# Kernel tuning notes

Hardware: AMD Instinct MI355X
Metric: run time of the kernel (lower is better)

## Reference

```python
import jax, jax.numpy as jnp
import numpy as np

B, N, D_OBJ, D_Q, D_FUSED, D_BOX, D_ATT = 64, 36, 2048, 2048, 2048, 4, 512


def setup_inputs() -> dict:
    key = jax.random.key(0)
    ks = jax.random.split(key, 12)
    s = lambda d: 1.0 / np.sqrt(d)
    return {
        "question_embedding": jax.random.normal(ks[0], (B * N, D_Q), jnp.float32),
        "object_features_list": jax.random.normal(ks[1], (B, N, D_OBJ), jnp.float32),
        "bounding_boxes": jax.random.uniform(ks[2], (B, N, D_BOX), jnp.float32),
        "Wq": jax.random.normal(ks[3], (D_Q, D_FUSED), jnp.float32) * s(D_Q),
        "Wo": jax.random.normal(ks[4], (D_OBJ, D_FUSED), jnp.float32) * s(D_OBJ),
        "Wfa": jax.random.normal(ks[5], (D_FUSED, D_FUSED), jnp.float32) * s(D_FUSED),
        "Wfb": jax.random.normal(ks[6], (D_FUSED, D_FUSED), jnp.float32) * s(D_FUSED),
        "Wba": jax.random.normal(ks[7], (D_BOX, D_FUSED), jnp.float32) * s(D_BOX),
        "Wbb": jax.random.normal(ks[8], (D_BOX, D_FUSED), jnp.float32) * s(D_BOX),
        "W0": jax.random.normal(ks[9], (D_FUSED, D_ATT), jnp.float32) * s(D_FUSED),
        "b0": jnp.zeros((D_ATT,), jnp.float32),
        "W1": jax.random.normal(ks[10], (D_ATT, 1), jnp.float32) * s(D_ATT),
        "b1": jnp.zeros((1,), jnp.float32),
        "batch_size": B,
        "num_obj": N,
    }


def reference(question_embedding, object_features_list, bounding_boxes,
              Wq, Wo, Wfa, Wfb, Wba, Wbb, W0, b0, W1, b1,
              batch_size, num_obj):
    # fuse_object_features_with_questions: MLB fusion of question and objects
    obj_flat = object_features_list.reshape(batch_size * num_obj, -1)  # [BN, D]
    fused = (question_embedding @ Wq) * (obj_flat @ Wo)                # [BN, Df]
    fused = fused.reshape(batch_size, num_obj, -1)                     # [B, N, Df]

    # pairwise: project once, broadcast-multiply instead of materializing
    # expanded [B*N*N, D] operands (same math as expand+view+fusion).
    ra = fused @ Wfa                 # [B, N, Df]
    rb = fused @ Wfb                 # [B, N, Df]
    ba = bounding_boxes @ Wba        # [B, N, Df]
    bb = bounding_boxes @ Wbb        # [B, N, Df]
    # relations[b, i, j, :] = fusion_fused(f_i, f_j) + fusion_box(box_i, box_j)
    relations = ra[:, :, None, :] * rb[:, None, :, :] + ba[:, :, None, :] * bb[:, None, :, :]  # [B,N,N,Df]

    # compute_relation_attention: linear-tanh-linear, softmax over dim=2
    h = jnp.tanh(relations @ W0 + b0)          # [B, N, N, D_att]
    scores = h @ W1 + b1                       # [B, N, N, 1]
    att = jax.nn.softmax(scores, axis=2)[..., 0]  # [B, N, N]
    e_hat = jnp.sum(relations * att[..., None], axis=2)  # [B, N, Df]

    pairwise_res = fused + e_hat
    return object_features_list + pairwise_res
```

## Files before the change

kernel.cpp:

```cpp
#include <hip/hip_runtime.h>
#include <hip/hip_bf16.h>
#include <math.h>

constexpr int kB    = 64;
constexpr int kN    = 36;
constexpr int kBN   = kB * kN;
constexpr int kD    = 2048;
constexpr int kDatt = 512;
constexpr int kPairs = kN * kN;

using bf16x8 = __attribute__((ext_vector_type(8))) short;
using f32x4  = __attribute__((ext_vector_type(4))) float;

typedef unsigned int u32;
typedef __attribute__((address_space(3))) u32 lds_u32;
typedef const __attribute__((address_space(1))) u32 glb_u32;

__device__ inline unsigned short f2bf(float f) {
    union { float f; unsigned u; } v; v.f = f;
    unsigned r = v.u + 0x7FFFu + ((v.u >> 16) & 1u);
    return (unsigned short)(r >> 16);
}

__global__ __launch_bounds__(256)
void kcvt(const float* __restrict__ x, unsigned short* __restrict__ y, int n4)
{
    int i = blockIdx.x * 256 + threadIdx.x;
    if (i < n4) {
        float4 v = ((const float4*)x)[i];
        ushort4 o = {f2bf(v.x), f2bf(v.y), f2bf(v.z), f2bf(v.w)};
        ((ushort4*)y)[i] = o;
    }
}

__global__ __launch_bounds__(256)
void kzero(float* __restrict__ p, int n)
{
    int i = blockIdx.x * 256 + threadIdx.x;
    if (i < n) p[i] = 0.f;
}

__global__ __launch_bounds__(256)
void ktrp(const float* __restrict__ W, unsigned short* __restrict__ WT, int nt)
{
    __shared__ float T[64][65];
    const int k0 = blockIdx.x * 64;
    const int n0 = blockIdx.y * 64;
    const int c = threadIdx.x & 63, r0 = threadIdx.x >> 6;
    #pragma unroll
    for (int rr = 0; rr < 64; rr += 4)
        T[r0 + rr][c] = W[(size_t)(k0 + r0 + rr) * nt + n0 + c];
    __syncthreads();
    #pragma unroll
    for (int rr = 0; rr < 64; rr += 4)
        WT[(size_t)(n0 + r0 + rr) * kD + k0 + c] = f2bf(T[c][r0 + rr]);
}

__global__ __launch_bounds__(64)
void krepack_w0(const unsigned short* __restrict__ W0T, unsigned short* __restrict__ W0s)
{
    const int kb    = blockIdx.x;
    const int chunk = blockIdx.y;
    const int g     = threadIdx.x;
    const int row = chunk * 16 + (g & 7) + ((g >> 5) << 3);
    const int cg8 = ((g >> 3) & 3) * 8;
    const uint4 v = *(const uint4*)&W0T[(size_t)row * kD + kb * 32 + cg8];
    *(uint4*)&W0s[(size_t)kb * 16384 + chunk * 512 + g * 8] = v;
}

__global__ __launch_bounds__(256)
void kgbox(const float* __restrict__ Wba, const float* __restrict__ Wbb,
           const float* __restrict__ W0, float* __restrict__ Gpart)
{
    __shared__ float red[4][64][17];
    const int ct = blockIdx.x;
    const int kc = blockIdx.y;
    const int cl = threadIdx.x & 63;
    const int kq = threadIdx.x >> 6;
    const int c  = ct * 64 + cl;

    float acc[16];
    #pragma unroll
    for (int t = 0; t < 16; ++t) acc[t] = 0.f;

    const int kbase = kc * 128 + kq * 32;
    for (int kk = 0; kk < 32; ++kk) {
        int k = kbase + kk;
        float w0 = W0[(size_t)k * kDatt + c];
        float a0 = Wba[k], a1 = Wba[kD + k], a2 = Wba[2 * kD + k], a3 = Wba[3 * kD + k];
        float b0 = Wbb[k] * w0, b1 = Wbb[kD + k] * w0,
              b2 = Wbb[2 * kD + k] * w0, b3 = Wbb[3 * kD + k] * w0;
        acc[0]  = fmaf(a0, b0, acc[0]);  acc[1]  = fmaf(a0, b1, acc[1]);
        acc[2]  = fmaf(a0, b2, acc[2]);  acc[3]  = fmaf(a0, b3, acc[3]);
        acc[4]  = fmaf(a1, b0, acc[4]);  acc[5]  = fmaf(a1, b1, acc[5]);
        acc[6]  = fmaf(a1, b2, acc[6]);  acc[7]  = fmaf(a1, b3, acc[7]);
        acc[8]  = fmaf(a2, b0, acc[8]);  acc[9]  = fmaf(a2, b1, acc[9]);
        acc[10] = fmaf(a2, b2, acc[10]); acc[11] = fmaf(a2, b3, acc[11]);
        acc[12] = fmaf(a3, b0, acc[12]); acc[13] = fmaf(a3, b1, acc[13]);
        acc[14] = fmaf(a3, b2, acc[14]); acc[15] = fmaf(a3, b3, acc[15]);
    }
    #pragma unroll
    for (int t = 0; t < 16; ++t) red[kq][cl][t] = acc[t];
    __syncthreads();
    #pragma unroll
    for (int t = 0; t < 4; ++t) {
        int s = threadIdx.x + t * 256;
        int cc = s >> 4, uv = s & 15;
        float v = red[0][cc][uv] + red[1][cc][uv] + red[2][cc][uv] + red[3][cc][uv];
        Gpart[((size_t)kc * 16 + uv) * kDatt + ct * 64 + cc] = v;
    }
}

__global__ __launch_bounds__(64)
void krepack_g(const float* __restrict__ Gpart, unsigned short* __restrict__ W0s)
{
    const int chunk = blockIdx.x;
    const int g     = threadIdx.x;
    const int col = chunk * 16 + (g & 7) + ((g >> 5) << 3);
    const int kg  = (g >> 3) & 3;
    unsigned short o[8];
    #pragma unroll
    for (int e = 0; e < 8; ++e) {
        int kl = kg * 8 + e;
        if (kl < 16) {
            float s = 0.f;
            #pragma unroll
            for (int kc = 0; kc < 16; ++kc)
                s += Gpart[((size_t)kc * 16 + kl) * kDatt + col];
            o[e] = f2bf(s);
        } else o[e] = 0;
    }
    *(uint4*)&W0s[(size_t)64 * 16384 + chunk * 512 + g * 8] = *(uint4*)o;
}

__device__ inline void stage128(const unsigned short* __restrict__ g,
                                int grow0, int k0,
                                unsigned short* lds, int w, int lane)
{
    const int sr = lane >> 2, sc = (lane & 3) * 8;
    #pragma unroll
    for (int t = 0; t < 2; ++t) {
        int r = w * 32 + t * 16;
        const unsigned short* gp = g + (size_t)(grow0 + r + sr) * kD + k0 + sc;
        __builtin_amdgcn_global_load_lds((glb_u32*)gp, (lds_u32*)(lds + r * 32), 16, 0, 0);
    }
}
__device__ inline void stage64(const unsigned short* __restrict__ g,
                               int grow0, int k0,
                               unsigned short* lds, int w, int lane)
{
    const int sr = lane >> 2, sc = (lane & 3) * 8;
    int r = w * 16;
    const unsigned short* gp = g + (size_t)(grow0 + r + sr) * kD + k0 + sc;
    __builtin_amdgcn_global_load_lds((glb_u32*)gp, (lds_u32*)(lds + r * 32), 16, 0, 0);
}

__global__ __launch_bounds__(256, 2)
void k1_dual_mfma(const unsigned short* __restrict__ Qb,
                  const unsigned short* __restrict__ WqT,
                  const unsigned short* __restrict__ Ob,
                  const unsigned short* __restrict__ WoT,
                  unsigned short* __restrict__ fusedb)
{
    __shared__ __align__(16) unsigned short As1[128][32];
    __shared__ __align__(16) unsigned short As2[128][32];
    __shared__ __align__(16) unsigned short Bs1[64][32];
    __shared__ __align__(16) unsigned short Bs2[64][32];

    const int tid = threadIdx.x;
    const int lane = tid & 63;
    const int w = tid >> 6;
    const int wm = w >> 1, wn = w & 1;
    const int row0 = blockIdx.y * 128;
    const int col0 = blockIdx.x * 64;

    f32x4 acc1[4][2], acc2[4][2];
    #pragma unroll
    for (int mt = 0; mt < 4; ++mt)
        #pragma unroll
        for (int nt = 0; nt < 2; ++nt) { acc1[mt][nt] = (f32x4)(0.f); acc2[mt][nt] = (f32x4)(0.f); }

    const int fr = lane & 15, ko = (lane >> 4) * 8;

    for (int k0 = 0; k0 < kD; k0 += 32) {
        stage128(Qb,  row0, k0, &As1[0][0], w, lane);
        stage128(Ob,  row0, k0, &As2[0][0], w, lane);
        stage64 (WqT, col0, k0, &Bs1[0][0], w, lane);
        stage64 (WoT, col0, k0, &Bs2[0][0], w, lane);
        __syncthreads();

        bf16x8 a1[4], a2[4];
        #pragma unroll
        for (int mt = 0; mt < 4; ++mt) {
            a1[mt] = *(bf16x8*)&As1[wm * 64 + mt * 16 + fr][ko];
            a2[mt] = *(bf16x8*)&As2[wm * 64 + mt * 16 + fr][ko];
        }
        #pragma unroll
        for (int nt = 0; nt < 2; ++nt) {
            bf16x8 b1 = *(bf16x8*)&Bs1[wn * 32 + nt * 16 + fr][ko];
            bf16x8 b2 = *(bf16x8*)&Bs2[wn * 32 + nt * 16 + fr][ko];
            #pragma unroll
            for (int mt = 0; mt < 4; ++mt) {
                acc1[mt][nt] = __builtin_amdgcn_mfma_f32_16x16x32_bf16(a1[mt], b1, acc1[mt][nt], 0, 0, 0);
                acc2[mt][nt] = __builtin_amdgcn_mfma_f32_16x16x32_bf16(a2[mt], b2, acc2[mt][nt], 0, 0, 0);
            }
        }
        __syncthreads();
    }

    const int fq = lane >> 4;
    #pragma unroll
    for (int mt = 0; mt < 4; ++mt)
        #pragma unroll
        for (int nt = 0; nt < 2; ++nt) {
            int row = row0 + wm * 64 + mt * 16 + fq * 4;
            int col = col0 + wn * 32 + nt * 16 + fr;
            #pragma unroll
            for (int reg = 0; reg < 4; ++reg) {
                float v = acc1[mt][nt][reg] * acc2[mt][nt][reg];
                fusedb[(size_t)(row + reg) * kD + col] = f2bf(v);
            }
        }
}

__global__ __launch_bounds__(256, 2)
void k2_dual_mfma(const unsigned short* __restrict__ Fb,
                  const unsigned short* __restrict__ WfaT,
                  const unsigned short* __restrict__ WfbT,
                  float* __restrict__ ra, float* __restrict__ rb)
{
    __shared__ __align__(16) unsigned short As [128][32];
    __shared__ __align__(16) unsigned short Bs1[64][32];
    __shared__ __align__(16) unsigned short Bs2[64][32];

    const int tid = threadIdx.x;
    const int lane = tid & 63;
    const int w = tid >> 6;
    const int wm = w >> 1, wn = w & 1;
    const int row0 = blockIdx.y * 128;
    const int col0 = blockIdx.x * 64;

    f32x4 acc1[4][2], acc2[4][2];
    #pragma unroll
    for (int mt = 0; mt < 4; ++mt)
        #pragma unroll
        for (int nt = 0; nt < 2; ++nt) { acc1[mt][nt] = (f32x4)(0.f); acc2[mt][nt] = (f32x4)(0.f); }

    const int fr = lane & 15, ko = (lane >> 4) * 8;

    for (int k0 = 0; k0 < kD; k0 += 32) {
        stage128(Fb,   row0, k0, &As [0][0], w, lane);
        stage64 (WfaT, col0, k0, &Bs1[0][0], w, lane);
        stage64 (WfbT, col0, k0, &Bs2[0][0], w, lane);
        __syncthreads();

        bf16x8 a[4];
        #pragma unroll
        for (int mt = 0; mt < 4; ++mt)
            a[mt] = *(bf16x8*)&As[wm * 64 + mt * 16 + fr][ko];
        #pragma unroll
        for (int nt = 0; nt < 2; ++nt) {
            bf16x8 b1 = *(bf16x8*)&Bs1[wn * 32 + nt * 16 + fr][ko];
            bf16x8 b2 = *(bf16x8*)&Bs2[wn * 32 + nt * 16 + fr][ko];
            #pragma unroll
            for (int mt = 0; mt < 4; ++mt) {
                acc1[mt][nt] = __builtin_amdgcn_mfma_f32_16x16x32_bf16(a[mt], b1, acc1[mt][nt], 0, 0, 0);
                acc2[mt][nt] = __builtin_amdgcn_mfma_f32_16x16x32_bf16(a[mt], b2, acc2[mt][nt], 0, 0, 0);
            }
        }
        __syncthreads();
    }

    const int fq = lane >> 4;
    #pragma unroll
    for (int mt = 0; mt < 4; ++mt)
        #pragma unroll
        for (int nt = 0; nt < 2; ++nt) {
            int row = row0 + wm * 64 + mt * 16 + fq * 4;
            int col = col0 + wn * 32 + nt * 16 + fr;
            #pragma unroll
            for (int reg = 0; reg < 4; ++reg) {
                size_t o = (size_t)(row + reg) * kD + col;
                ra[o] = acc1[mt][nt][reg];
                rb[o] = acc2[mt][nt][reg];
            }
        }
}

__global__ __launch_bounds__(512, 4)
void k4_scores_mfma(const float* __restrict__ ra, const float* __restrict__ rb,
                    const float* __restrict__ box,
                    const unsigned short* __restrict__ W0s,
                    const float* __restrict__ b0, const float* __restrict__ W1,
                    float* __restrict__ scores)
{
    __shared__ __align__(16) unsigned short Bs[2][256 * 32];
    __shared__ __align__(16) unsigned short RelS[2][128][40];
    __shared__ __align__(16) float4 Stg4[2][378];
    __shared__ float scoreS[128];

    const int tid  = threadIdx.x;
    const int lane = tid & 63;
    const int w    = tid >> 6;
    const int wm   = w >> 2;
    const int wn   = w & 3;

    const int work = (blockIdx.x & 7) * 176 + (blockIdx.x >> 3);
    const int colb = work & 1;
    const int wt   = work >> 1;
    const int b    = wt / 11;
    const int tile = wt - b * 11;
    const int p0   = tile * 128;
    const int i0   = p0 / kN;

    const float* raB  = ra  + (size_t)b * kN * kD;
    const float* rbB  = rb  + (size_t)b * kN * kD;
    const float* boxB = box + (size_t)b * kN * 4;

    const bool hasStage = (tid < 336);
    const float* sptr;
    int sdst;
    {
        int s = hasStage ? tid : 335;
        int row = s >> 3, q = s & 7;
        int grow; const float* base;
        if (row < 6) {
            int il = (row < 5) ? row : 4;
            grow = i0 + il; if (grow > kN - 1) grow = kN - 1;
            base = raB;
        } else {
            grow = row - 6;
            base = rbB;
        }
        sptr = base + (size_t)grow * kD + q * 4;
        sdst = row * 9 + q;
    }

    int rowA, cg2, iA, jA, sA, sR;
    {
        rowA = tid >> 2; cg2 = tid & 3;
        int p = p0 + rowA; if (p >= kPairs) p = kPairs - 1;
        iA = p / kN;
        jA = p - iA * kN;
        int ilA = iA - i0;
        sA = ilA * 9 + cg2 * 2;
        sR = (6 + jA) * 9 + cg2 * 2;
    }

    const int fr = lane & 15, fq = lane >> 4;
    const int bco = ((fr & 7) << 3) + ((fr >> 3) << 8) + (fq << 6);

    f32x4 acc[4][4];
    #pragma unroll
    for (int mt = 0; mt < 4; ++mt)
        #pragma unroll
        for (int nt = 0; nt < 4; ++nt)
            acc[mt][nt] = (f32x4)(0.f);

    if (tid < 128) scoreS[tid] = 0.f;

    float4 sreg0;

    #define ISSUE_B(k0_, buf_)                                                   \
        _Pragma("unroll")                                                        \
        for (int t = 0; t < 2; ++t) {                                            \
            int ch = w * 2 + t;                                                  \
            const unsigned short* gp = W0s + (size_t)((k0_) >> 5) * 16384        \
                                       + (colb * 16 + ch) * 512 + lane * 8;      \
            __builtin_amdgcn_global_load_lds((glb_u32*)gp,                       \
                (lds_u32*)&Bs[buf_][ch * 512], 16, 0, 0);                        \
        }

    #define STAGE_LOAD(k0_) {                                                    \
            if (hasStage) sreg0 = *(const float4*)(sptr + (k0_));                \
        }

    #define STAGE_WRITE(buf_) {                                                  \
            if (hasStage) Stg4[buf_][sdst] = sreg0;                              \
        }

    #define REL_GEN(buf_) {                                                      \
            float4 va0 = Stg4[buf_][sA],     va1 = Stg4[buf_][sA + 1];           \
            float4 vr0 = Stg4[buf_][sR],     vr1 = Stg4[buf_][sR + 1];           \
            unsigned short o[8];                                                 \
            o[0] = f2bf(va0.x * vr0.x); o[1] = f2bf(va0.y * vr0.y);              \
            o[2] = f2bf(va0.z * vr0.z); o[3] = f2bf(va0.w * vr0.w);              \
            o[4] = f2bf(va1.x * vr1.x); o[5] = f2bf(va1.y * vr1.y);              \
            o[6] = f2bf(va1.z * vr1.z); o[7] = f2bf(va1.w * vr1.w);              \
            *(bf16x8*)&RelS[buf_][rowA][cg2 * 8] = *(bf16x8*)o;                  \
        }

    #define REL_GEN_BOX(buf_) {                                                  \
            unsigned short o[8] = {0, 0, 0, 0, 0, 0, 0, 0};                      \
            if (cg2 < 2) {                                                       \
                float4 bj = *(const float4*)(boxB + jA * 4);                     \
                float biu0 = boxB[iA * 4 + cg2 * 2];                             \
                float biu1 = boxB[iA * 4 + cg2 * 2 + 1];                         \
                o[0] = f2bf(biu0 * bj.x); o[1] = f2bf(biu0 * bj.y);              \
                o[2] = f2bf(biu0 * bj.z); o[3] = f2bf(biu0 * bj.w);              \
                o[4] = f2bf(biu1 * bj.x); o[5] = f2bf(biu1 * bj.y);              \
                o[6] = f2bf(biu1 * bj.z); o[7] = f2bf(biu1 * bj.w);              \
            }                                                                    \
            *(bf16x8*)&RelS[buf_][rowA][cg2 * 8] = *(bf16x8*)o;                  \
        }

    STAGE_LOAD(0)
    STAGE_WRITE(0)
    STAGE_LOAD(32)
    __syncthreads();
    REL_GEN(0)
    STAGE_WRITE(1)
    ISSUE_B(0, 0)

    for (int k = 0; k <= 64; ++k) {
        const int cur = k & 1, nxt = cur ^ 1;
        __syncthreads();
        if (k < 62) STAGE_LOAD((k + 2) * 32)
        if (k < 64) ISSUE_B((k + 1) * 32, nxt)
        bf16x8 af[4];
        #pragma unroll
        for (int mt = 0; mt < 4; ++mt)
            af[mt] = *(bf16x8*)&RelS[cur][wm * 64 + mt * 16 + fr][fq * 8];
        if (k < 63) REL_GEN(nxt)
        else if (k == 63) REL_GEN_BOX(nxt)
        __builtin_amdgcn_s_setprio(1);
        #pragma unroll
        for (int nt = 0; nt < 4; ++nt) {
            bf16x8 bfv = *(bf16x8*)&Bs[cur][wn * 2048 + nt * 512 + bco];
            #pragma unroll
            for (int mt = 0; mt < 4; ++mt)
                acc[mt][nt] = __builtin_amdgcn_mfma_f32_16x16x32_bf16(af[mt], bfv, acc[mt][nt], 0, 0, 0);
        }
        __builtin_amdgcn_s_setprio(0);
        if (k < 62) STAGE_WRITE(cur)
    }

    float b0v[4], w1v[4];
    #pragma unroll
    for (int nt = 0; nt < 4; ++nt) {
        int col = colb * 256 + wn * 64 + nt * 16 + fr;
        b0v[nt] = b0[col];
        w1v[nt] = W1[col];
    }
    #pragma unroll
    for (int mt = 0; mt < 4; ++mt) {
        #pragma unroll
        for (int reg = 0; reg < 4; ++reg) {
            float p = 0.f;
            #pragma unroll
            for (int nt = 0; nt < 4; ++nt)
                p += w1v[nt] * tanhf(acc[mt][nt][reg] + b0v[nt]);
            p += __shfl_xor(p, 1, 64);
            p += __shfl_xor(p, 2, 64);
            p += __shfl_xor(p, 4, 64);
            p += __shfl_xor(p, 8, 64);
            if (fr == 0)
                atomicAdd(&scoreS[wm * 64 + mt * 16 + fq * 4 + reg], p);
        }
    }
    __syncthreads();
    if (tid < 128 && p0 + tid < kPairs)
        atomicAdd(&scores[(size_t)b * kPairs + p0 + tid], scoreS[tid]);
}

__global__ __launch_bounds__(64)
void k5_softmax(const float* __restrict__ scores, const float* __restrict__ box,
                float* __restrict__ att, float* __restrict__ abox)
{
    const int bi = blockIdx.x;
    const int b  = bi / kN;
    const int tid = threadIdx.x;
    float s = (tid < kN) ? scores[(size_t)bi * kN + tid] : -1e30f;
    float m = s;
    #pragma unroll
    for (int off = 32; off >= 1; off >>= 1)
        m = fmaxf(m, __shfl_xor(m, off, 64));
    float e = (tid < kN) ? expf(s - m) : 0.f;
    float sum = e;
    #pragma unroll
    for (int off = 32; off >= 1; off >>= 1)
        sum += __shfl_xor(sum, off, 64);
    float a = e / sum;
    if (tid < kN) att[(size_t)bi * kN + tid] = a;

    float4 bx = {0.f, 0.f, 0.f, 0.f};
    if (tid < kN) bx = *(const float4*)(box + (size_t)(b * kN + tid) * 4);
    bx.x *= a; bx.y *= a; bx.z *= a; bx.w *= a;
    #pragma unroll
    for (int off = 32; off >= 1; off >>= 1) {
        bx.x += __shfl_xor(bx.x, off, 64);
        bx.y += __shfl_xor(bx.y, off, 64);
        bx.z += __shfl_xor(bx.z, off, 64);
        bx.w += __shfl_xor(bx.w, off, 64);
    }
    if (tid == 0) *(float4*)(abox + (size_t)bi * 4) = bx;
}

__global__ __launch_bounds__(256)
void k6_output(const float* __restrict__ obj, const unsigned short* __restrict__ fusedb,
               const float* __restrict__ ra, const float* __restrict__ rb,
               const float* __restrict__ att, const float* __restrict__ box,
               const float* __restrict__ abox,
               const float* __restrict__ Wba, const float* __restrict__ Wbb,
               float* __restrict__ out)
{
    __shared__ float attS[kN];
    const int bi = blockIdx.x;
    const int b = bi / kN;
    const int tid = threadIdx.x;
    if (tid < kN) attS[tid] = att[(size_t)bi * kN + tid];
    __syncthreads();
    const float4 bxi = *(const float4*)(box  + (size_t)bi * 4);
    const float4 axi = *(const float4*)(abox + (size_t)bi * 4);
    for (int d = tid; d < kD; d += 256) {
        float s1 = 0.f;
        #pragma unroll 4
        for (int j = 0; j < kN; ++j)
            s1 = fmaf(attS[j], rb[(size_t)(b * kN + j) * kD + d], s1);
        float bav = bxi.x * Wba[d] + bxi.y * Wba[kD + d]
                  + bxi.z * Wba[2 * kD + d] + bxi.w * Wba[3 * kD + d];
        float s2  = axi.x * Wbb[d] + axi.y * Wbb[kD + d]
                  + axi.z * Wbb[2 * kD + d] + axi.w * Wbb[3 * kD + d];
        size_t o = (size_t)bi * kD + d;
        float fv = __uint_as_float((u32)fusedb[o] << 16);
        out[o] = obj[o] + fv + ra[o] * s1 + bav * s2;
    }
}

extern "C" void kernel_launch(void* const* d_in, const int* in_sizes, int n_in,
                              void* d_out, int out_size, void* d_ws, size_t ws_size,
                              hipStream_t stream)
{
    const float* q   = (const float*)d_in[0];
    const float* obj = (const float*)d_in[1];
    const float* box = (const float*)d_in[2];
    const float* Wq  = (const float*)d_in[3];
    const float* Wo  = (const float*)d_in[4];
    const float* Wfa = (const float*)d_in[5];
    const float* Wfb = (const float*)d_in[6];
    const float* Wba = (const float*)d_in[7];
    const float* Wbb = (const float*)d_in[8];
    const float* W0  = (const float*)d_in[9];
    const float* b0v = (const float*)d_in[10];
    const float* W1  = (const float*)d_in[11];
    float* out = (float*)d_out;

    const size_t nBD = (size_t)kBN * kD;
    float* ws = (float*)d_ws;
    size_t off = 0;
    float* ra     = ws + off; off += nBD;
    float* rb     = ws + off; off += nBD;
    float* scores = ws + off; off += (size_t)kBN * kN;
    float* att    = ws + off; off += (size_t)kBN * kN;
    float* abox   = ws + off; off += (size_t)kBN * 4;
    float* Gpart  = ws + off; off += (size_t)16 * 16 * kDatt;

    unsigned short* us = (unsigned short*)(ws + off);
    size_t uoff = 0;
    unsigned short* W0T     = us + uoff; uoff += (size_t)kDatt * kD;
    unsigned short* W0s     = us + uoff; uoff += (size_t)65 * 16384;
    unsigned short* q_bf    = us + uoff; uoff += nBD;
    unsigned short* obj_bf  = us + uoff; uoff += nBD;
    unsigned short* fusedbf = us + uoff; uoff += nBD;
    unsigned short* WqT     = us + uoff; uoff += (size_t)kD * kD;
    unsigned short* WoT     = us + uoff; uoff += (size_t)kD * kD;
    unsigned short* WfaT = q_bf;
    unsigned short* WfbT = obj_bf;

    const int n4 = (int)(nBD / 4);
    kcvt<<<dim3((n4 + 255) / 256), 256, 0, stream>>>(q,   q_bf,   n4);
    kcvt<<<dim3((n4 + 255) / 256), 256, 0, stream>>>(obj, obj_bf, n4);
    ktrp<<<dim3(32, 32), 256, 0, stream>>>(Wq, WqT, kD);
    ktrp<<<dim3(32, 32), 256, 0, stream>>>(Wo, WoT, kD);
    ktrp<<<dim3(32, 8),  256, 0, stream>>>(W0, W0T, kDatt);
    krepack_w0<<<dim3(kD / 32, kDatt / 16), 64, 0, stream>>>(W0T, W0s);
    kgbox<<<dim3(8, 16), 256, 0, stream>>>(Wba, Wbb, W0, Gpart);
    krepack_g<<<dim3(32), 64, 0, stream>>>(Gpart, W0s);
    kzero<<<dim3((kBN * kN + 255) / 256), 256, 0, stream>>>(scores, kBN * kN);

    k1_dual_mfma<<<dim3(kD / 64, kBN / 128), 256, 0, stream>>>(q_bf, WqT, obj_bf, WoT, fusedbf);

    ktrp<<<dim3(32, 32), 256, 0, stream>>>(Wfa, WfaT, kD);
    ktrp<<<dim3(32, 32), 256, 0, stream>>>(Wfb, WfbT, kD);

    k2_dual_mfma<<<dim3(kD / 64, kBN / 128), 256, 0, stream>>>(fusedbf, WfaT, WfbT, ra, rb);

    k4_scores_mfma<<<dim3(kB * 11 * 2), 512, 0, stream>>>(ra, rb, box, W0s, b0v, W1, scores);
    k5_softmax<<<kBN, 64, 0, stream>>>(scores, box, att, abox);
    k6_output<<<kBN, 256, 0, stream>>>(obj, fusedbf, ra, rb, att, box, abox, Wba, Wbb, out);
}
```

Baseline: 645.7 us.

## Pre-tile GEMM operands into MFMA fragment order for contiguous LDS staging

The bf16 conversion and weight-transpose kernels now write activations and weights in a tiled layout of [k-block][16-row chunk][fragment-ordered 512 elements]. Each global_load_lds in the two dual GEMMs then moves one fully contiguous 1KB chunk, and LDS reads use a fixed in-chunk offset instead of row-strided addressing. This is meant to improve global coalescing and avoid LDS bank conflicts. The fused output is stored in the same tiled layout, so the output kernel reads it with scattered 2-byte loads, and that kernel's block-to-row mapping is also permuted.

Result: faster. 622.9 us (-3.5%).

```diff
diff --git a/kernel.cpp b/kernel.cpp
--- a/kernel.cpp
+++ b/kernel.cpp
@@ -16,6 +16,7 @@
 typedef __attribute__((address_space(3))) u32 lds_u32;
 typedef const __attribute__((address_space(1))) u32 glb_u32;
 
+
 __device__ inline unsigned short f2bf(float f) {
     union { float f; unsigned u; } v; v.f = f;
     unsigned r = v.u + 0x7FFFu + ((v.u >> 16) & 1u);
@@ -23,14 +24,18 @@
 }
 
 __global__ __launch_bounds__(256)
-void kcvt(const float* __restrict__ x, unsigned short* __restrict__ y, int n4)
+void kcvt_t(const float* __restrict__ x, unsigned short* __restrict__ y)
 {
     int i = blockIdx.x * 256 + threadIdx.x;
-    if (i < n4) {
-        float4 v = ((const float4*)x)[i];
-        ushort4 o = {f2bf(v.x), f2bf(v.y), f2bf(v.z), f2bf(v.w)};
-        ((ushort4*)y)[i] = o;
-    }
+    if (i >= kBN * (kD / 4)) return;
+    float4 v = ((const float4*)x)[i];
+    ushort4 o = {f2bf(v.x), f2bf(v.y), f2bf(v.z), f2bf(v.w)};
+    int row = i >> 9;
+    int kf  = (i & 511) << 2;
+    int kb = kf >> 5;
+    int chunk = row >> 4, rl = row & 15;
+    int g = (rl & 7) | (((kf >> 3) & 3) << 3) | ((rl >> 3) << 5);
+    *(ushort4*)&y[(size_t)kb * (144 * 512) + chunk * 512 + g * 8 + (kf & 7)] = o;
 }
 
 __global__ __launch_bounds__(256)
@@ -54,6 +59,28 @@
     #pragma unroll
     for (int rr = 0; rr < 64; rr += 4)
         WT[(size_t)(n0 + r0 + rr) * kD + k0 + c] = f2bf(T[c][r0 + rr]);
+}
+
+__global__ __launch_bounds__(256)
+void ktrp_t(const float* __restrict__ W, unsigned short* __restrict__ Wt)
+{
+    __shared__ float T[64][65];
+    const int k0 = blockIdx.x * 64;
+    const int n0 = blockIdx.y * 64;
+    const int c = threadIdx.x & 63, r0 = threadIdx.x >> 6;
+    #pragma unroll
+    for (int rr = 0; rr < 64; rr += 4)
+        T[r0 + rr][c] = W[(size_t)(k0 + r0 + rr) * kD + n0 + c];
+    __syncthreads();
+    #pragma unroll
+    for (int rr = 0; rr < 64; rr += 4) {
+        int row = n0 + r0 + rr;
+        int k   = k0 + c;
+        int kb = k >> 5, kl = k & 31;
+        int chunk = row >> 4, rl = row & 15;
+        int g = (rl & 7) | (((kl >> 3) & 3) << 3) | ((rl >> 3) << 5);
+        Wt[(size_t)kb * (128 * 512) + chunk * 512 + g * 8 + (kl & 7)] = f2bf(T[c][r0 + rr]);
+    }
 }
 
 __global__ __launch_bounds__(64)
@@ -133,39 +160,17 @@
     *(uint4*)&W0s[(size_t)64 * 16384 + chunk * 512 + g * 8] = *(uint4*)o;
 }
 
-__device__ inline void stage128(const unsigned short* __restrict__ g,
-                                int grow0, int k0,
-                                unsigned short* lds, int w, int lane)
-{
-    const int sr = lane >> 2, sc = (lane & 3) * 8;
-    #pragma unroll
-    for (int t = 0; t < 2; ++t) {
-        int r = w * 32 + t * 16;
-        const unsigned short* gp = g + (size_t)(grow0 + r + sr) * kD + k0 + sc;
-        __builtin_amdgcn_global_load_lds((glb_u32*)gp, (lds_u32*)(lds + r * 32), 16, 0, 0);
-    }
-}
-__device__ inline void stage64(const unsigned short* __restrict__ g,
-                               int grow0, int k0,
-                               unsigned short* lds, int w, int lane)
-{
-    const int sr = lane >> 2, sc = (lane & 3) * 8;
-    int r = w * 16;
-    const unsigned short* gp = g + (size_t)(grow0 + r + sr) * kD + k0 + sc;
-    __builtin_amdgcn_global_load_lds((glb_u32*)gp, (lds_u32*)(lds + r * 32), 16, 0, 0);
-}
-
 __global__ __launch_bounds__(256, 2)
-void k1_dual_mfma(const unsigned short* __restrict__ Qb,
-                  const unsigned short* __restrict__ WqT,
-                  const unsigned short* __restrict__ Ob,
-                  const unsigned short* __restrict__ WoT,
-                  unsigned short* __restrict__ fusedb)
-{
-    __shared__ __align__(16) unsigned short As1[128][32];
-    __shared__ __align__(16) unsigned short As2[128][32];
-    __shared__ __align__(16) unsigned short Bs1[64][32];
-    __shared__ __align__(16) unsigned short Bs2[64][32];
+void k1_dual_mfma(const unsigned short* __restrict__ Qt,
+                  const unsigned short* __restrict__ Wqt,
+                  const unsigned short* __restrict__ Ot,
+                  const unsigned short* __restrict__ Wot,
+                  unsigned short* __restrict__ fusedt)
+{
+    __shared__ __align__(16) unsigned short As1[128 * 32];
+    __shared__ __align__(16) unsigned short As2[128 * 32];
+    __shared__ __align__(16) unsigned short Bs1[64 * 32];
+    __shared__ __align__(16) unsigned short Bs2[64 * 32];
 
     const int tid = threadIdx.x;
     const int lane = tid & 63;
@@ -173,6 +178,8 @@
     const int wm = w >> 1, wn = w & 1;
     const int row0 = blockIdx.y * 128;
     const int col0 = blockIdx.x * 64;
+    const int chA = row0 >> 4;
+    const int chB = col0 >> 4;
 
     f32x4 acc1[4][2], acc2[4][2];
     #pragma unroll
@@ -180,25 +187,34 @@
         #pragma unroll
         for (int nt = 0; nt < 2; ++nt) { acc1[mt][nt] = (f32x4)(0.f); acc2[mt][nt] = (f32x4)(0.f); }
 
-    const int fr = lane & 15, ko = (lane >> 4) * 8;
-
-    for (int k0 = 0; k0 < kD; k0 += 32) {
-        stage128(Qb,  row0, k0, &As1[0][0], w, lane);
-        stage128(Ob,  row0, k0, &As2[0][0], w, lane);
-        stage64 (WqT, col0, k0, &Bs1[0][0], w, lane);
-        stage64 (WoT, col0, k0, &Bs2[0][0], w, lane);
+    const int fr = lane & 15, fq = lane >> 4;
+    const int inoff = ((fr & 7) << 3) | (fq << 6) | ((fr >> 3) << 8);
+
+    for (int kb = 0; kb < 64; ++kb) {
+        #pragma unroll
+        for (int t = 0; t < 2; ++t) {
+            int cl = w * 2 + t;
+            __builtin_amdgcn_global_load_lds((glb_u32*)(Qt + ((size_t)kb * 144 + chA + cl) * 512 + lane * 8),
+                                             (lds_u32*)&As1[cl * 512], 16, 0, 0);
+            __builtin_amdgcn_global_load_lds((glb_u32*)(Ot + ((size_t)kb * 144 + chA + cl) * 512 + lane * 8),
+                                             (lds_u32*)&As2[cl * 512], 16, 0, 0);
+        }
+        __builtin_amdgcn_global_load_lds((glb_u32*)(Wqt + ((size_t)kb * 128 + chB + w) * 512 + lane * 8),
+                                         (lds_u32*)&Bs1[w * 512], 16, 0, 0);
+        __builtin_amdgcn_global_load_lds((glb_u32*)(Wot + ((size_t)kb * 128 + chB + w) * 512 + lane * 8),
+                                         (lds_u32*)&Bs2[w * 512], 16, 0, 0);
         __syncthreads();
 
         bf16x8 a1[4], a2[4];
         #pragma unroll
         for (int mt = 0; mt < 4; ++mt) {
-            a1[mt] = *(bf16x8*)&As1[wm * 64 + mt * 16 + fr][ko];
-            a2[mt] = *(bf16x8*)&As2[wm * 64 + mt * 16 + fr][ko];
+            a1[mt] = *(bf16x8*)&As1[(wm * 4 + mt) * 512 + inoff];
+            a2[mt] = *(bf16x8*)&As2[(wm * 4 + mt) * 512 + inoff];
         }
         #pragma unroll
         for (int nt = 0; nt < 2; ++nt) {
-            bf16x8 b1 = *(bf16x8*)&Bs1[wn * 32 + nt * 16 + fr][ko];
-            bf16x8 b2 = *(bf16x8*)&Bs2[wn * 32 + nt * 16 + fr][ko];
+            bf16x8 b1 = *(bf16x8*)&Bs1[(wn * 2 + nt) * 512 + inoff];
+            bf16x8 b2 = *(bf16x8*)&Bs2[(wn * 2 + nt) * 512 + inoff];
             #pragma unroll
             for (int mt = 0; mt < 4; ++mt) {
                 acc1[mt][nt] = __builtin_amdgcn_mfma_f32_16x16x32_bf16(a1[mt], b1, acc1[mt][nt], 0, 0, 0);
@@ -208,30 +224,32 @@
         __syncthreads();
     }
 
-    const int fq = lane >> 4;
     #pragma unroll
     for (int mt = 0; mt < 4; ++mt)
         #pragma unroll
         for (int nt = 0; nt < 2; ++nt) {
-            int row = row0 + wm * 64 + mt * 16 + fq * 4;
-            int col = col0 + wn * 32 + nt * 16 + fr;
             #pragma unroll
             for (int reg = 0; reg < 4; ++reg) {
+                int row = row0 + wm * 64 + mt * 16 + fq * 4 + reg;
+                int col = col0 + wn * 32 + nt * 16 + fr;
                 float v = acc1[mt][nt][reg] * acc2[mt][nt][reg];
-                fusedb[(size_t)(row + reg) * kD + col] = f2bf(v);
+                int kbo = col >> 5, kl = col & 31;
+                int chunk = row >> 4, rl = row & 15;
+                int g = (rl & 7) | (((kl >> 3) & 3) << 3) | ((rl >> 3) << 5);
+                fusedt[(size_t)kbo * (144 * 512) + chunk * 512 + g * 8 + (kl & 7)] = f2bf(v);
             }
         }
 }
 
 __global__ __launch_bounds__(256, 2)
-void k2_dual_mfma(const unsigned short* __restrict__ Fb,
-                  const unsigned short* __restrict__ WfaT,
-                  const unsigned short* __restrict__ WfbT,
+void k2_dual_mfma(const unsigned short* __restrict__ Ft,
+                  const unsigned short* __restrict__ Wfat,
+                  const unsigned short* __restrict__ Wfbt,
                   float* __restrict__ ra, float* __restrict__ rb)
 {
-    __shared__ __align__(16) unsigned short As [128][32];
-    __shared__ __align__(16) unsigned short Bs1[64][32];
-    __shared__ __align__(16) unsigned short Bs2[64][32];
+    __shared__ __align__(16) unsigned short As [128 * 32];
+    __shared__ __align__(16) unsigned short Bs1[64 * 32];
+    __shared__ __align__(16) unsigned short Bs2[64 * 32];
 
     const int tid = threadIdx.x;
     const int lane = tid & 63;
@@ -239,6 +257,8 @@
     const int wm = w >> 1, wn = w & 1;
     const int row0 = blockIdx.y * 128;
     const int col0 = blockIdx.x * 64;
+    const int chA = row0 >> 4;
+    const int chB = col0 >> 4;
 
     f32x4 acc1[4][2], acc2[4][2];
     #pragma unroll
@@ -246,22 +266,30 @@
         #pragma unroll
         for (int nt = 0; nt < 2; ++nt) { acc1[mt][nt] = (f32x4)(0.f); acc2[mt][nt] = (f32x4)(0.f); }
 
-    const int fr = lane & 15, ko = (lane >> 4) * 8;
-
-    for (int k0 = 0; k0 < kD; k0 += 32) {
-        stage128(Fb,   row0, k0, &As [0][0], w, lane);
-        stage64 (WfaT, col0, k0, &Bs1[0][0], w, lane);
-        stage64 (WfbT, col0, k0, &Bs2[0][0], w, lane);
+    const int fr = lane & 15, fq = lane >> 4;
+    const int inoff = ((fr & 7) << 3) | (fq << 6) | ((fr >> 3) << 8);
+
+    for (int kb = 0; kb < 64; ++kb) {
+        #pragma unroll
+        for (int t = 0; t < 2; ++t) {
+            int cl = w * 2 + t;
+            __builtin_amdgcn_global_load_lds((glb_u32*)(Ft + ((size_t)kb * 144 + chA + cl) * 512 + lane * 8),
+                                             (lds_u32*)&As[cl * 512], 16, 0, 0);
+        }
+        __builtin_amdgcn_global_load_lds((glb_u32*)(Wfat + ((size_t)kb * 128 + chB + w) * 512 + lane * 8),
+                                         (lds_u32*)&Bs1[w * 512], 16, 0, 0);
+        __builtin_amdgcn_global_load_lds((glb_u32*)(Wfbt + ((size_t)kb * 128 + chB + w) * 512 + lane * 8),
+                                         (lds_u32*)&Bs2[w * 512], 16, 0, 0);
         __syncthreads();
 
         bf16x8 a[4];
         #pragma unroll
         for (int mt = 0; mt < 4; ++mt)
-            a[mt] = *(bf16x8*)&As[wm * 64 + mt * 16 + fr][ko];
+            a[mt] = *(bf16x8*)&As[(wm * 4 + mt) * 512 + inoff];
         #pragma unroll
         for (int nt = 0; nt < 2; ++nt) {
-            bf16x8 b1 = *(bf16x8*)&Bs1[wn * 32 + nt * 16 + fr][ko];
-            bf16x8 b2 = *(bf16x8*)&Bs2[wn * 32 + nt * 16 + fr][ko];
+            bf16x8 b1 = *(bf16x8*)&Bs1[(wn * 2 + nt) * 512 + inoff];
+            bf16x8 b2 = *(bf16x8*)&Bs2[(wn * 2 + nt) * 512 + inoff];
             #pragma unroll
             for (int mt = 0; mt < 4; ++mt) {
                 acc1[mt][nt] = __builtin_amdgcn_mfma_f32_16x16x32_bf16(a[mt], b1, acc1[mt][nt], 0, 0, 0);
@@ -271,7 +299,6 @@
         __syncthreads();
     }
 
-    const int fq = lane >> 4;
     #pragma unroll
     for (int mt = 0; mt < 4; ++mt)
         #pragma unroll
@@ -497,7 +524,7 @@
 }
 
 __global__ __launch_bounds__(256)
-void k6_output(const float* __restrict__ obj, const unsigned short* __restrict__ fusedb,
+void k6_output(const float* __restrict__ obj, const unsigned short* __restrict__ fusedt,
                const float* __restrict__ ra, const float* __restrict__ rb,
                const float* __restrict__ att, const float* __restrict__ box,
                const float* __restrict__ abox,
@@ -505,13 +532,14 @@
                float* __restrict__ out)
 {
     __shared__ float attS[kN];
-    const int bi = blockIdx.x;
+    const int bi = (blockIdx.x & 7) * 288 + (blockIdx.x >> 3);
     const int b = bi / kN;
     const int tid = threadIdx.x;
     if (tid < kN) attS[tid] = att[(size_t)bi * kN + tid];
     __syncthreads();
     const float4 bxi = *(const float4*)(box  + (size_t)bi * 4);
     const float4 axi = *(const float4*)(abox + (size_t)bi * 4);
+    const int chunk = bi >> 4, rl = bi & 15;
     for (int d = tid; d < kD; d += 256) {
         float s1 = 0.f;
         #pragma unroll 4
@@ -522,7 +550,10 @@
         float s2  = axi.x * Wbb[d] + axi.y * Wbb[kD + d]
                   + axi.z * Wbb[2 * kD + d] + axi.w * Wbb[3 * kD + d];
         size_t o = (size_t)bi * kD + d;
-        float fv = __uint_as_float((u32)fusedb[o] << 16);
+        int kbf = d >> 5, klf = d & 31;
+        int g = (rl & 7) | (((klf >> 3) & 3) << 3) | ((rl >> 3) << 5);
+        float fv = __uint_as_float(
+            (u32)fusedt[(size_t)kbf * (144 * 512) + chunk * 512 + g * 8 + (klf & 7)] << 16);
         out[o] = obj[o] + fv + ra[o] * s1 + bav * s2;
     }
 }
@@ -557,35 +588,34 @@
 
     unsigned short* us = (unsigned short*)(ws + off);
     size_t uoff = 0;
-    unsigned short* W0T     = us + uoff; uoff += (size_t)kDatt * kD;
-    unsigned short* W0s     = us + uoff; uoff += (size_t)65 * 16384;
-    unsigned short* q_bf    = us + uoff; uoff += nBD;
-    unsigned short* obj_bf  = us + uoff; uoff += nBD;
-    unsigned short* fusedbf = us + uoff; uoff += nBD;
-    unsigned short* WqT     = us + uoff; uoff += (size_t)kD * kD;
-    unsigned short* WoT     = us + uoff; uoff += (size_t)kD * kD;
-    unsigned short* WfaT = q_bf;
-    unsigned short* WfbT = obj_bf;
-
-    const int n4 = (int)(nBD / 4);
-    kcvt<<<dim3((n4 + 255) / 256), 256, 0, stream>>>(q,   q_bf,   n4);
-    kcvt<<<dim3((n4 + 255) / 256), 256, 0, stream>>>(obj, obj_bf, n4);
-    ktrp<<<dim3(32, 32), 256, 0, stream>>>(Wq, WqT, kD);
-    ktrp<<<dim3(32, 32), 256, 0, stream>>>(Wo, WoT, kD);
-    ktrp<<<dim3(32, 8),  256, 0, stream>>>(W0, W0T, kDatt);
-    krepack_w0<<<dim3(kD / 32, kDatt / 16), 64, 0, stream>>>(W0T, W0s);
+    unsigned short* W0T    = us + uoff; uoff += (size_t)kDatt * kD;
+    unsigned short* W0s    = us + uoff; uoff += (size_t)65 * 16384;
+    unsigned short* qt     = us + uoff; uoff += nBD;
+    unsigned short* objt   = us + uoff; uoff += nBD;
+    unsigned short* fusedt = us + uoff; uoff += nBD;
+    unsigned short* Wqt    = us + uoff; uoff += (size_t)kD * kD;
+    unsigned short* Wot    = us + uoff; uoff += (size_t)kD * kD;
+    unsigned short* Wfat = qt;
+    unsigned short* Wfbt = objt;
+
+    kcvt_t<<<dim3(kBN * (kD / 4) / 256), 256, 0, stream>>>(q,   qt);
+    kcvt_t<<<dim3(kBN * (kD / 4) / 256), 256, 0, stream>>>(obj, objt);
+    ktrp<<<dim3(32, 8), 256, 0, stream>>>(W0, W0T, kDatt);
+    krepack_w0<<<dim3(64, 32), 64, 0, stream>>>(W0T, W0s);
     kgbox<<<dim3(8, 16), 256, 0, stream>>>(Wba, Wbb, W0, Gpart);
     krepack_g<<<dim3(32), 64, 0, stream>>>(Gpart, W0s);
     kzero<<<dim3((kBN * kN + 255) / 256), 256, 0, stream>>>(scores, kBN * kN);
-
-    k1_dual_mfma<<<dim3(kD / 64, kBN / 128), 256, 0, stream>>>(q_bf, WqT, obj_bf, WoT, fusedbf);
-
-    ktrp<<<dim3(32, 32), 256, 0, stream>>>(Wfa, WfaT, kD);
-    ktrp<<<dim3(32, 32), 256, 0, stream>>>(Wfb, WfbT, kD);
-
-    k2_dual_mfma<<<dim3(kD / 64, kBN / 128), 256, 0, stream>>>(fusedbf, WfaT, WfbT, ra, rb);
+    ktrp_t<<<dim3(32, 32), 256, 0, stream>>>(Wq, Wqt);
+    ktrp_t<<<dim3(32, 32), 256, 0, stream>>>(Wo, Wot);
+
+    k1_dual_mfma<<<dim3(kD / 64, kBN / 128), 256, 0, stream>>>(qt, Wqt, objt, Wot, fusedt);
+
+    ktrp_t<<<dim3(32, 32), 256, 0, stream>>>(Wfa, Wfat);
+    ktrp_t<<<dim3(32, 32), 256, 0, stream>>>(Wfb, Wfbt);
+
+    k2_dual_mfma<<<dim3(kD / 64, kBN / 128), 256, 0, stream>>>(fusedt, Wfat, Wfbt, ra, rb);
 
     k4_scores_mfma<<<dim3(kB * 11 * 2), 512, 0, stream>>>(ra, rb, box, W0s, b0v, W1, scores);
     k5_softmax<<<kBN, 64, 0, stream>>>(scores, box, att, abox);
-    k6_output<<<kBN, 256, 0, stream>>>(obj, fusedbf, ra, rb, att, box, abox, Wba, Wbb, out);
-}
+    k6_output<<<kBN, 256, 0, stream>>>(obj, fusedt, ra, rb, att, box, abox, Wba, Wbb, out);
+}
```
